# Optimization experiments

Hardware: AMD Instinct MI355X
Metric: run time of the kernel (lower is better)

## Reference

```python
import jax, jax.numpy as jnp
import numpy as np
from jax import lax

S = 101; MAX_LEN = 100; MIN_LEN = 5; NEG = -1e4

def _build_constraints():
    t = np.zeros((S, S), bool)
    t[0, 0] = True; t[0, 1] = True
    for i in range(1, MAX_LEN):
        if i < MAX_LEN - 1:
            t[i, i + 1] = True
        if i >= MIN_LEN - 1:
            t[i, MAX_LEN] = True
    t[MAX_LEN - 1, MAX_LEN - 1] = True; t[MAX_LEN - 1, MAX_LEN] = True
    t[MAX_LEN, 0] = True; t[MAX_LEN, 1] = True
    s = np.ones(S, bool)
    e = np.zeros(S, bool); e[0] = True; e[MAX_LEN] = True
    return jnp.array(t), jnp.array(s), jnp.array(e)

T_ALLOW, S_ALLOW, E_ALLOW = _build_constraints()

def pos_encoding(L, D):
    pos = jnp.arange(L, dtype=jnp.float32)[:, None]
    div = jnp.exp(jnp.arange(0, D, 2, dtype=jnp.float32) * (-np.log(10000.0) / D))
    ang = pos * div
    return jnp.stack([jnp.sin(ang), jnp.cos(ang)], -1).reshape(L, D)

def layernorm(x, g, b, eps=1e-5):
    m = jnp.mean(x, -1, keepdims=True)
    v = jnp.var(x, -1, keepdims=True)
    return (x - m) / jnp.sqrt(v + eps) * g + b

def conv1d(x, w, b):
    # x: (B,C,L), w: (O,I,K), 'same' padding
    k = w.shape[-1]
    y = lax.conv_general_dilated(x, w, (1,), [(k // 2, k // 2)], dimension_numbers=("NCH", "OIH", "NCH"))
    return y + b[None, :, None]

def lstm(x, Wih, Whh, bih, bhh, reverse):
    # x: (B,L,F). PyTorch gate order i,f,g,o.
    B = x.shape[0]; H = Whh.shape[1]
    xs = jnp.swapaxes(x, 0, 1) @ Wih.T + (bih + bhh)  # (L,B,4H)
    def step(carry, xt):
        h, c = carry
        g = xt + h @ Whh.T
        i, f, gg, o = jnp.split(g, 4, axis=-1)
        c = jax.nn.sigmoid(f) * c + jax.nn.sigmoid(i) * jnp.tanh(gg)
        h = jax.nn.sigmoid(o) * jnp.tanh(c)
        return (h, c), h
    h0 = jnp.zeros((B, H), x.dtype)
    _, hs = lax.scan(step, (h0, h0), xs, reverse=reverse)
    return jnp.swapaxes(hs, 0, 1)

def crf_marginals(emis, trans, start, end):
    # forward-backward in log space; mask is all ones (full length)
    ex = jnp.swapaxes(emis, 0, 1)  # (L,B,S)
    a0 = start + ex[0]
    def fstep(a, e):
        a2 = jax.nn.logsumexp(a[:, :, None] + trans[None], axis=1) + e
        return a2, a2
    _, al = lax.scan(fstep, a0, ex[1:])
    alphas = jnp.concatenate([a0[None], al], 0)  # (L,B,S)
    logZ = jax.nn.logsumexp(alphas[-1] + end, axis=-1)  # (B,)
    bT = jnp.broadcast_to(end, a0.shape)
    def bstep(b, e):
        b2 = jax.nn.logsumexp(trans[None] + (e + b)[:, None, :], axis=2)
        return b2, b2
    _, bt = lax.scan(bstep, bT, ex[1:], reverse=True)
    betas = jnp.concatenate([bt, bT[None]], 0)
    probs = jax.nn.softmax(alphas + betas, axis=-1)  # logsumexp(alpha+beta)=logZ
    return jnp.swapaxes(probs, 0, 1), logZ

def viterbi(emis, trans, start, end, logZ):
    ex = jnp.swapaxes(emis, 0, 1)  # (L,B,S)
    v0 = start + ex[0]
    def vstep(v, e):
        sc = v[:, :, None] + trans[None]  # (B,S,S)
        return jnp.max(sc, 1) + e, jnp.argmax(sc, 1).astype(jnp.int32)
    vT, ptrs = lax.scan(vstep, v0, ex[1:])
    fin = vT + end
    last = jnp.argmax(fin, -1).astype(jnp.int32)
    best = jnp.max(fin, -1)
    def back(st, p):
        prev = jnp.take_along_axis(p, st[:, None], axis=1)[:, 0]
        return prev, prev
    _, rest = lax.scan(back, last, ptrs, reverse=True)
    path = jnp.concatenate([rest, last[None]], 0)  # (L,B)
    return jnp.swapaxes(path, 0, 1), jnp.exp(best - logZ)

def features_to_emissions(embeddings, W_bneck, b_bneck, ln_g, ln_b, conv1_w, conv1_b, Wih_f, Whh_f, bih_f, bhh_f, Wih_b, Whh_b, bih_b, bhh_b, conv2_w, conv2_b, W_emis, b_emis):
    B, D, L = embeddings.shape
    x = jnp.swapaxes(embeddings, 1, 2) + pos_encoding(L, D)  # (B,L,D)
    x = jax.nn.relu(layernorm(x @ W_bneck + b_bneck, ln_g, ln_b))
    x = jax.nn.relu(conv1d(jnp.swapaxes(x, 1, 2), conv1_w, conv1_b))
    x = jnp.swapaxes(x, 1, 2)  # (B,L,64)
    h = jnp.concatenate([lstm(x, Wih_f, Whh_f, bih_f, bhh_f, False),
                         lstm(x, Wih_b, Whh_b, bih_b, bhh_b, True)], -1)  # (B,L,256)
    feats = jnp.swapaxes(jax.nn.relu(conv1d(jnp.swapaxes(h, 1, 2), conv2_w, conv2_b)), 1, 2)  # (B,L,128)
    e = feats @ W_emis + b_emis  # (B,L,2); propeptide_bias = 0.0
    # _repeat_emissions: state 0 <- label 0, states 1..100 <- label 1
    return jnp.concatenate([e[..., 0:1], jnp.broadcast_to(e[..., 1:2], (B, L, MAX_LEN))], -1)

def setup_inputs():
    key = jax.random.key(0)
    ks = jax.random.split(key, 16)
    B, L, D = 32, 1024, 1536
    C, F, H, NL = 256, 64, 128, 2
    rn = lambda k, sh, s: s * jax.random.normal(k, sh, jnp.float32)
    return {
        "embeddings": jax.random.normal(ks[0], (B, D, L), jnp.float32),
        "mask": jnp.ones((B, L), jnp.int32),
        "top_k": 1,
        "W_bneck": rn(ks[1], (D, C), 0.02), "b_bneck": jnp.zeros((C,)),
        "ln_g": jnp.ones((C,)), "ln_b": jnp.zeros((C,)),
        "conv1_w": rn(ks[2], (F, C, 3), 0.05), "conv1_b": jnp.zeros((F,)),
        "Wih_f": rn(ks[3], (4 * H, F), 0.08), "Whh_f": rn(ks[4], (4 * H, H), 0.08),
        "bih_f": jnp.zeros((4 * H,)), "bhh_f": jnp.zeros((4 * H,)),
        "Wih_b": rn(ks[5], (4 * H, F), 0.08), "Whh_b": rn(ks[6], (4 * H, H), 0.08),
        "bih_b": jnp.zeros((4 * H,)), "bhh_b": jnp.zeros((4 * H,)),
        "conv2_w": rn(ks[7], (2 * F, 2 * H, 5), 0.04), "conv2_b": jnp.zeros((2 * F,)),
        "W_emis": rn(ks[8], (2 * F, NL), 0.1), "b_emis": jnp.zeros((NL,)),
        "crf_trans": rn(ks[9], (S, S), 0.1),
        "crf_start": rn(ks[10], (S,), 0.1),
        "crf_end": rn(ks[11], (S,), 0.1),
    }

def reference(embeddings, mask, top_k, W_bneck, b_bneck, ln_g, ln_b, conv1_w, conv1_b, Wih_f, Whh_f, bih_f, bhh_f, Wih_b, Whh_b, bih_b, bhh_b, conv2_w, conv2_b, W_emis, b_emis, crf_trans, crf_start, crf_end):
    # mask is all-ones -> packed LSTM == plain LSTM; top_k == 1 Viterbi.
    emis = features_to_emissions(embeddings, W_bneck, b_bneck, ln_g, ln_b, conv1_w, conv1_b, Wih_f, Whh_f, bih_f, bhh_f, Wih_b, Whh_b, bih_b, bhh_b, conv2_w, conv2_b, W_emis, b_emis)
    trans = jnp.where(T_ALLOW, crf_trans, NEG)
    start = jnp.where(S_ALLOW, crf_start, NEG)
    end = jnp.where(E_ALLOW, crf_end, NEG)
    probs, logZ = crf_marginals(emis, trans, start, end)
    paths, path_probs = viterbi(emis, trans, start, end, logZ)
    return probs, paths, path_probs
```

## Files before the change

kernel.cpp:

```cpp
#include <hip/hip_runtime.h>
#include <cstdint>
#include <cstddef>

#define BB 32
#define LL 1024
#define DD 1536
#define SS 101
#define NEGV (-1e4f)
#define NINF (-1e30f)
#define L2E 1.4426950408889634f
#define LN2 0.6931471805599453f

#define NPE   (1024*1536)
#define NX2   (32768*256)
#define NX3   (32768*64)
#define NG    (32768*512)
#define NF2   (32768*128)
#define NEM   (32768*101)

#define OFF_PE    0
#define OFF_X2    (OFF_PE + NPE)
#define OFF_X3    (OFF_X2 + NX2)
#define OFF_GF    (OFF_X3 + NX3)
#define OFF_GB    (OFF_GF + NG)
#define OFF_F2    (OFF_GF)
#define OFF_EMIS  (OFF_GF + NF2)
#define OFF_ALPHA (OFF_EMIS + NEM)
#define OFF_LOGZ  (OFF_ALPHA + NEM)
#define OFF_VBEST (OFF_LOGZ + 64)
#define OFF_WT_F  (OFF_GB + NG)
#define OFF_WT_B  (OFF_WT_F + 32768)
#define OFF_BS_F  (OFF_WT_B + 32768)
#define OFF_BS_B  (OFF_BS_F + 512)
#define OFF_W1R   (OFF_BS_B + 512)
#define OFF_W2R   (OFF_W1R + 49152)

#define LDS_BARRIER asm volatile("s_waitcnt lgkmcnt(0)\ns_barrier" ::: "memory")

__global__ __launch_bounds__(256)
void prep_k(const float* __restrict__ Wihf, const float* __restrict__ Wihb,
            const float* __restrict__ bihf, const float* __restrict__ bhhf,
            const float* __restrict__ bihb, const float* __restrict__ bhhb,
            const float* __restrict__ w1, const float* __restrict__ w2,
            float* __restrict__ ws)
{
  int idx = blockIdx.x * 256 + threadIdx.x;
  if (idx < NPE) {
    int k = idx >> 10, l = idx & 1023;
    int j2 = (k >> 1) * 2;
    float freq = expf((float)j2 * (-9.210340371976184f / 1536.f));
    float ang = (float)l * freq;
    ws[OFF_PE + idx] = (k & 1) ? cosf(ang) : sinf(ang);
    return;
  }
  idx -= NPE;
  if (idx < 32768) { int k = idx >> 9, n = idx & 511; ws[OFF_WT_F + idx] = Wihf[n*64 + k]; return; }
  idx -= 32768;
  if (idx < 32768) { int k = idx >> 9, n = idx & 511; ws[OFF_WT_B + idx] = Wihb[n*64 + k]; return; }
  idx -= 32768;
  if (idx < 512) { ws[OFF_BS_F + idx] = bihf[idx] + bhhf[idx]; return; }
  idx -= 512;
  if (idx < 512) { ws[OFF_BS_B + idx] = bihb[idx] + bhhb[idx]; return; }
  idx -= 512;
  if (idx < 49152) {
    int f = idx & 63, tc = idx >> 6;
    int t = tc >> 8, c = tc & 255;
    ws[OFF_W1R + idx] = w1[(f*256 + c)*3 + t];
    return;
  }
  idx -= 49152;
  if (idx < 163840) {
    int f = idx & 127, tc = idx >> 7;
    int t = tc >> 8, c = tc & 255;
    ws[OFF_W2R + idx] = w2[(f*256 + c)*5 + t];
  }
}

template<int BM, int BN, int AMODE, int PADT, bool RELU>
__global__ __launch_bounds__(256)
void gemm_tpl(const float* __restrict__ Ap, const float* __restrict__ Bp,
              const float* __restrict__ biasp, float* __restrict__ Cp,
              const float* __restrict__ PEp, const float* __restrict__ EMBp,
              int M, int N, int K, int lda)
{
  constexpr int BK = 16;
  __shared__ __align__(16) float As[BK][BM + 4];
  __shared__ __align__(16) float Bs[BK][BN];
  constexpr int TX = BN / 8, TY = BM / 8;
  const int tid = threadIdx.x;
  const int tx = tid % TX, ty = tid / TX;
  const int m0 = blockIdx.x * BM;
  const int n0 = blockIdx.y * BN;
  float acc[8][8];
  #pragma unroll
  for (int i = 0; i < 8; i++)
    #pragma unroll
    for (int j = 0; j < 8; j++) acc[i][j] = 0.f;

  for (int k0 = 0; k0 < K; k0 += BK) {
    if constexpr (AMODE == 0) {
      #pragma unroll
      for (int i = 0; i < (BK*BM)/256; ++i) {
        int e = tid + i*256;
        int ml = e % BM, kk = e / BM;
        int row = m0 + ml; int b = row >> 10; int l = row & 1023;
        int k = k0 + kk;
        As[kk][ml] = EMBp[((size_t)b*DD + k)*LL + l] + PEp[(size_t)k*LL + l];
      }
    } else {
      #pragma unroll
      for (int i = 0; i < (BK*BM)/256; ++i) {
        int e = tid + i*256;
        int kk = e % BK, ml = e / BK;
        int row = m0 + ml; int k = k0 + kk;
        float v;
        if constexpr (AMODE == 1) {
          v = Ap[(size_t)row*lda + k];
        } else {
          int c = k & 255, t = k >> 8;
          int l = row & 1023, sl = l + t - PADT;
          v = ((unsigned)sl < 1024u) ? Ap[(size_t)(row + t - PADT)*lda + c] : 0.f;
        }
        As[kk][ml] = v;
      }
    }
    #pragma unroll
    for (int i = 0; i < (BK*BN)/256; ++i) {
      int e = tid + i*256;
      int nl = e % BN, kk = e / BN;
      Bs[kk][nl] = Bp[(size_t)(k0+kk)*N + n0 + nl];
    }
    __syncthreads();
    #pragma unroll
    for (int k = 0; k < BK; ++k) {
      float4 a0 = *(const float4*)&As[k][ty*4];
      float4 a1 = *(const float4*)&As[k][BM/2 + ty*4];
      float4 b0 = *(const float4*)&Bs[k][tx*4];
      float4 b1 = *(const float4*)&Bs[k][BN/2 + tx*4];
      float av[8] = {a0.x,a0.y,a0.z,a0.w,a1.x,a1.y,a1.z,a1.w};
      float bv[8] = {b0.x,b0.y,b0.z,b0.w,b1.x,b1.y,b1.z,b1.w};
      #pragma unroll
      for (int i = 0; i < 8; i++)
        #pragma unroll
        for (int j = 0; j < 8; j++) acc[i][j] += av[i]*bv[j];
    }
    __syncthreads();
  }
  float4 bias0 = *(const float4*)&biasp[n0 + tx*4];
  float4 bias1 = *(const float4*)&biasp[n0 + BN/2 + tx*4];
  float bn[8] = {bias0.x,bias0.y,bias0.z,bias0.w,bias1.x,bias1.y,bias1.z,bias1.w};
  #pragma unroll
  for (int i = 0; i < 8; i++) {
    int r = m0 + ((i < 4) ? (ty*4 + i) : (BM/2 + ty*4 + i - 4));
    float o[8];
    #pragma unroll
    for (int j = 0; j < 8; j++) {
      float v = acc[i][j] + bn[j];
      o[j] = RELU ? fmaxf(v, 0.f) : v;
    }
    *(float4*)&Cp[(size_t)r*N + n0 + tx*4] = make_float4(o[0],o[1],o[2],o[3]);
    *(float4*)&Cp[(size_t)r*N + n0 + BN/2 + tx*4] = make_float4(o[4],o[5],o[6],o[7]);
  }
}

__global__ __launch_bounds__(256)
void ln_relu_k(float* __restrict__ X, const float* __restrict__ g, const float* __restrict__ bt)
{
  const int lane = threadIdx.x & 63, wv = threadIdx.x >> 6;
  const size_t row = (size_t)blockIdx.x * 4 + wv;
  float4 v = *(const float4*)&X[row*256 + lane*4];
  float s = v.x + v.y + v.z + v.w;
  float q = v.x*v.x + v.y*v.y + v.z*v.z + v.w*v.w;
  #pragma unroll
  for (int d = 1; d < 64; d <<= 1) { s += __shfl_xor(s, d); q += __shfl_xor(q, d); }
  float mean = s * (1.f/256.f);
  float var = q * (1.f/256.f) - mean*mean;
  float inv = 1.f / sqrtf(var + 1e-5f);
  float4 gg = *(const float4*)&g[lane*4];
  float4 bb = *(const float4*)&bt[lane*4];
  float4 o;
  o.x = fmaxf(0.f, (v.x-mean)*inv*gg.x + bb.x);
  o.y = fmaxf(0.f, (v.y-mean)*inv*gg.y + bb.y);
  o.z = fmaxf(0.f, (v.z-mean)*inv*gg.z + bb.z);
  o.w = fmaxf(0.f, (v.w-mean)*inv*gg.w + bb.w);
  *(float4*)&X[row*256 + lane*4] = o;
}

__device__ __forceinline__ float fast_sigmoid(float x){
  return 1.f / (1.f + exp2f(-x * L2E));
}
__device__ __forceinline__ float fast_tanh(float x){
  return 1.f - 2.f / (exp2f(x * (2.f * L2E)) + 1.f);
}

__global__ __launch_bounds__(512)
void lstm_k(const float* __restrict__ GF, const float* __restrict__ GB,
            const float* __restrict__ WhhF, const float* __restrict__ WhhB,
            float* __restrict__ Hcat)
{
  const int dir = blockIdx.y;
  const int b = blockIdx.x;
  const int j = threadIdx.x;
  const float* G = dir ? GB : GF;
  const float* Whh = dir ? WhhB : WhhF;
  float w[128];
  #pragma unroll
  for (int i = 0; i < 32; ++i) {
    float4 t4 = *(const float4*)&Whh[(size_t)j*128 + i*4];
    w[4*i+0] = t4.x; w[4*i+1] = t4.y; w[4*i+2] = t4.z; w[4*i+3] = t4.w;
  }
  __shared__ __align__(16) float hs[128];
  __shared__ float gs[512];
  if (j < 128) hs[j] = 0.f;
  float c = 0.f;
  const size_t gbase = (size_t)b * LL * 512 + j;
  float gcur = G[gbase + (size_t)(dir ? 1023 : 0) * 512];
  __syncthreads();
  for (int step = 0; step < LL; ++step) {
    const int l = dir ? (1023 - step) : step;
    float gnext = 0.f;
    if (step + 1 < LL) {
      const int ln = dir ? (1022 - step) : (step + 1);
      gnext = G[gbase + (size_t)ln * 512];
    }
    #pragma unroll
    for (int k = 0; k < 128; ++k)
      asm volatile("" : "+v"(w[k]));
    float ac0 = gcur, ac1 = 0.f, ac2 = 0.f, ac3 = 0.f;
    #pragma unroll
    for (int i = 0; i < 8; ++i) {
      float4 h0 = *(const float4*)&hs[16*i];
      float4 h1 = *(const float4*)&hs[16*i + 4];
      float4 h2 = *(const float4*)&hs[16*i + 8];
      float4 h3 = *(const float4*)&hs[16*i + 12];
      ac0 += h0.x*w[16*i]    + h0.y*w[16*i+1]  + h0.z*w[16*i+2]  + h0.w*w[16*i+3];
      ac1 += h1.x*w[16*i+4]  + h1.y*w[16*i+5]  + h1.z*w[16*i+6]  + h1.w*w[16*i+7];
      ac2 += h2.x*w[16*i+8]  + h2.y*w[16*i+9]  + h2.z*w[16*i+10] + h2.w*w[16*i+11];
      ac3 += h3.x*w[16*i+12] + h3.y*w[16*i+13] + h3.z*w[16*i+14] + h3.w*w[16*i+15];
    }
    float acc = (ac0 + ac1) + (ac2 + ac3);
    float gv = ((j >> 7) == 2) ? fast_tanh(acc) : fast_sigmoid(acc);
    gs[j] = gv;
    LDS_BARRIER;
    if (j < 128) {
      float ig = gs[j], fg = gs[128+j], g2 = gs[256+j], og = gs[384+j];
      c = fg*c + ig*g2;
      float hh = og * fast_tanh(c);
      hs[j] = hh;
      Hcat[((size_t)b*LL + l)*256 + (dir << 7) + j] = hh;
    }
    LDS_BARRIER;
    gcur = gnext;
  }
}

__device__ __forceinline__ float wave_sum_f(float v){
  #pragma unroll
  for (int d = 1; d < 64; d <<= 1) v += __shfl_xor(v, d);
  return v;
}
__device__ __forceinline__ float wave_max_f(float v){
  #pragma unroll
  for (int d = 1; d < 64; d <<= 1) v = fmaxf(v, __shfl_xor(v, d));
  return v;
}
__device__ __forceinline__ float rdlanef(float v, int l){
  union { float f; int i; } u; u.f = v;
  u.i = __builtin_amdgcn_readlane(u.i, l);
  return u.f;
}
__device__ __forceinline__ float lse2f(float x, float y){
  float mx = fmaxf(x, y), mn = fminf(x, y);
  return mx + log2f(1.f + exp2f((mn - mx) * L2E)) * LN2;
}

__global__ __launch_bounds__(256)
void emis_k(const float* __restrict__ F2, const float* __restrict__ W,
            const float* __restrict__ bias, float* __restrict__ EM)
{
  const int lane = threadIdx.x & 63;
  const size_t m = (size_t)blockIdx.x * 4 + (threadIdx.x >> 6);
  float f1 = F2[m*128 + lane], f2 = F2[m*128 + 64 + lane];
  float e0 = f1*W[lane*2]   + f2*W[(64+lane)*2];
  float e1 = f1*W[lane*2+1] + f2*W[(64+lane)*2+1];
  e0 = wave_sum_f(e0) + bias[0];
  e1 = wave_sum_f(e1) + bias[1];
  float* row = EM + m*SS;
  row[lane] = (lane == 0) ? e0 : e1;
  if (lane < 37) row[64 + lane] = e1;
}

__global__ __launch_bounds__(64)
void crf1_k(const float* __restrict__ EM, const float* __restrict__ T,
            const float* __restrict__ startv, const float* __restrict__ endv,
            float* __restrict__ AL, float* __restrict__ LOGZ,
            float* __restrict__ paths, float* __restrict__ vbest)
{
  __shared__ unsigned int lptr[LL];
  const int lane = threadIdx.x;
  const int s1 = lane, s2 = 64 + lane;
  const bool has2 = lane < 37;
  float ta1, tb1 = 0.f, tc1 = NINF, ta2 = 0.f, tb2 = 0.f, tc2 = NINF;
  if (s1 == 0)      { ta1 = T[0]; tb1 = T[100*101 + 0]; }
  else if (s1 == 1) { ta1 = T[1]; tb1 = T[100*101 + 1]; }
  else ta1 = T[(s1-1)*101 + s1];
  if (s1 >= 4) tc1 = T[s1*101 + 100];
  if (has2) {
    if (s2 <= 98) ta2 = T[(s2-1)*101 + s2];
    else if (s2 == 99) { ta2 = T[98*101 + 99]; tb2 = T[99*101 + 99]; }
    if (s2 <= 99) tc2 = T[s2*101 + 100];
  }

  if (blockIdx.x < 32) {
    const int b = blockIdx.x;
    const float* E = EM + (size_t)b*LL*SS;
    float* A = AL + (size_t)b*LL*SS;
    float a1 = startv[s1] + E[s1];
    float a2 = has2 ? (startv[s2] + E[s2]) : NINF;
    A[s1] = a1;
    if (has2) A[s2] = a2;
    float M;
    {
      float v1 = a1 + tc1;
      float v2 = a2 + tc2;
      M = wave_max_f(fmaxf(v1, v2));
    }
    auto fstep = [&](int l, float e1, float e2) {
      float v1 = a1 + tc1;
      float v2 = a2 + tc2;
      float p = exp2f((v1 - M) * L2E) + exp2f((v2 - M) * L2E);
      p = fmaxf(wave_sum_f(p), 1e-37f);
      float lse100 = M + log2f(p) * LN2;
      float a1m1 = __shfl_up(a1, 1);
      float a2m1 = __shfl_up(a2, 1);
      float a1t  = rdlanef(a1, 63);
      float a0s  = rdlanef(a1, 0);
      float a100 = rdlanef(a2, 36);
      float n1 = (s1 <= 1) ? lse2f(a0s + ta1, a100 + tb1) : (a1m1 + ta1);
      float n2;
      if (s2 == 64) n2 = a1t + ta2;
      else if (s2 <= 98) n2 = a2m1 + ta2;
      else if (s2 == 99) n2 = lse2f(a2m1 + ta2, a2 + tb2);
      else n2 = lse100;
      a1 = n1 + e1;
      a2 = has2 ? (n2 + e2) : NINF;
      float* Ar = A + (size_t)l*SS;
      Ar[s1] = a1;
      if (has2) Ar[s2] = a2;
      M = lse100;
    };
    int l = 1;
    for (; l + 3 < LL; l += 4) {
      float e1a[4], e2a[4];
      #pragma unroll
      for (int u = 0; u < 4; ++u) {
        const float* e = E + (size_t)(l+u)*SS;
        e1a[u] = e[s1]; e2a[u] = has2 ? e[s2] : 0.f;
      }
      #pragma unroll
      for (int u = 0; u < 4; ++u) fstep(l+u, e1a[u], e2a[u]);
    }
    for (; l < LL; ++l) {
      const float* e = E + (size_t)l*SS;
      fstep(l, e[s1], has2 ? e[s2] : 0.f);
    }
    float w1 = a1 + ((s1 == 0) ? endv[0] : NEGV);
    float w2 = has2 ? (a2 + ((s2 == 100) ? endv[100] : NEGV)) : NINF;
    float Mx = wave_max_f(fmaxf(w1, w2));
    float P = wave_sum_f(exp2f((w1 - Mx) * L2E) + exp2f((w2 - Mx) * L2E));
    if (lane == 0) LOGZ[b] = Mx + log2f(P) * LN2;
  } else {
    const int b = blockIdx.x - 32;
    const float* E = EM + (size_t)b*LL*SS;
    float v1 = startv[s1] + E[s1];
    float v2 = has2 ? (startv[s2] + E[s2]) : NINF;
    auto vstep = [&](int l, float e1, float e2) {
      float c1 = v1 + tc1;
      float c2 = v2 + tc2;
      float Mx = wave_max_f(fmaxf(c1, c2));
      unsigned long long m1 = __ballot(c1 == Mx);
      int bi;
      if (m1 != 0ULL) bi = __ffsll((unsigned long long)m1) - 1;
      else bi = 64 + __ffsll((unsigned long long)__ballot(c2 == Mx)) - 1;
      float v1m1 = __shfl_up(v1, 1);
      float v2m1 = __shfl_up(v2, 1);
      float v1t  = rdlanef(v1, 63);
      float v0s  = rdlanef(v1, 0);
      float v100 = rdlanef(v2, 36);
      float n1; int p1i;
      if (s1 <= 1) {
        float x0 = v0s + ta1, x1 = v100 + tb1;
        if (x1 > x0) { n1 = x1; p1i = 100; } else { n1 = x0; p1i = 0; }
      } else { n1 = v1m1 + ta1; p1i = s1 - 1; }
      float n2 = NINF; int p2i = 0;
      if (has2) {
        if (s2 == 64) { n2 = v1t + ta2; p2i = 63; }
        else if (s2 <= 98) { n2 = v2m1 + ta2; p2i = s2 - 1; }
        else if (s2 == 99) {
          float x98 = v2m1 + ta2, x99 = v2 + tb2;
          if (x99 > x98) { n2 = x99; p2i = 99; } else { n2 = x98; p2i = 98; }
        } else { n2 = Mx; p2i = bi; }
      }
      v1 = n1 + e1;
      v2 = has2 ? (n2 + e2) : NINF;
      int q0   = __builtin_amdgcn_readlane(p1i, 0);
      int q1   = __builtin_amdgcn_readlane(p1i, 1);
      int q99  = __builtin_amdgcn_readlane(p2i, 35);
      int q100 = __builtin_amdgcn_readlane(p2i, 36);
      if (lane == 0)
        lptr[l] = (unsigned)q0 | ((unsigned)q1 << 8) | ((unsigned)q99 << 16) | ((unsigned)q100 << 24);
    };
    int l = 1;
    for (; l + 3 < LL; l += 4) {
      float e1a[4], e2a[4];
      #pragma unroll
      for (int u = 0; u < 4; ++u) {
        const float* e = E + (size_t)(l+u)*SS;
        e1a[u] = e[s1]; e2a[u] = has2 ? e[s2] : 0.f;
      }
      #pragma unroll
      for (int u = 0; u < 4; ++u) vstep(l+u, e1a[u], e2a[u]);
    }
    for (; l < LL; ++l) {
      const float* e = E + (size_t)l*SS;
      vstep(l, e[s1], has2 ? e[s2] : 0.f);
    }
    float w1 = v1 + ((s1 == 0) ? endv[0] : NEGV);
    float w2 = has2 ? (v2 + ((s2 == 100) ? endv[100] : NEGV)) : NINF;
    float Mx = wave_max_f(fmaxf(w1, w2));
    unsigned long long m1 = __ballot(w1 == Mx);
    int last;
    if (m1 != 0ULL) last = __ffsll((unsigned long long)m1) - 1;
    else last = 64 + __ffsll((unsigned long long)__ballot(w2 == Mx)) - 1;
    if (lane == 0) vbest[b] = Mx;
    __syncthreads();
    float* po = paths + (size_t)b*LL;
    int st = last;
    for (int ch = 15; ch >= 0; --ch) {
      unsigned pk = lptr[ch*64 + lane];
      int myval = 0;
      #pragma unroll 1
      for (int j = 63; j >= 0; --j) {
        int t = ch*64 + j;
        if (t >= 1) {
          unsigned pp = __shfl((int)pk, j);
          int prev;
          if (st >= 2 && st <= 98) prev = st - 1;
          else if (st == 0)  prev = (int)(pp & 0xffu);
          else if (st == 1)  prev = (int)((pp >> 8) & 0xffu);
          else if (st == 99) prev = (int)((pp >> 16) & 0xffu);
          else               prev = (int)((pp >> 24) & 0xffu);
          if (j == lane) myval = prev;
          st = prev;
        }
      }
      int ii = ch*64 + lane;
      if (ii >= 1) po[ii - 1] = (float)myval;
    }
    if (lane == 0) po[1023] = (float)last;
  }
}

__global__ __launch_bounds__(64)
void crf_bwd_k(const float* __restrict__ EM, const float* __restrict__ AL,
               const float* __restrict__ T, const float* __restrict__ endv,
               float* __restrict__ U)
{
  const int b = blockIdx.x, lane = threadIdx.x;
  const int s1 = lane, s2 = 64 + lane;
  const bool has2 = lane < 37;
  const float* E = EM + (size_t)b*LL*SS;
  const float* A = AL + (size_t)b*LL*SS;
  float* PR = U + (size_t)b*LL*SS;
  float tn1 = T[s1*101 + s1 + 1];
  float tj1 = (s1 >= 4) ? T[s1*101 + 100] : 0.f;
  float tn2 = (has2 && s2 <= 99) ? T[s2*101 + s2 + 1] : 0.f;
  float tj2 = (has2 && s2 <= 98) ? T[s2*101 + 100] : 0.f;
  float t00 = T[0];
  float t9999 = T[99*101 + 99];
  float t100_0 = T[100*101 + 0], t100_1 = T[100*101 + 1];
  float b1 = (s1 == 0) ? endv[0] : NEGV;
  float b2 = has2 ? ((s2 == 100) ? endv[100] : NEGV) : NINF;
  PR[(size_t)1023*SS + s1] = A[(size_t)1023*SS + s1] + b1;
  if (has2) PR[(size_t)1023*SS + s2] = A[(size_t)1023*SS + s2] + b2;
  auto bstep = [&](int l, float e1, float e2, float a1r, float a2r) {
    float u1 = e1 + b1;
    float u2 = has2 ? (e2 + b2) : NINF;
    float un1 = __shfl_down(u1, 1);
    float un2 = __shfl_down(u2, 1);
    float u64v = rdlanef(u2, 0);
    float u99  = rdlanef(u2, 35);
    float u100 = rdlanef(u2, 36);
    float u0s  = rdlanef(u1, 0);
    float u1s  = rdlanef(u1, 1);
    float nb1;
    if (s1 == 0) nb1 = lse2f(t00 + u0s, tn1 + u1s);
    else if (s1 <= 3) nb1 = tn1 + un1;
    else if (s1 <= 62) nb1 = lse2f(tn1 + un1, tj1 + u100);
    else nb1 = lse2f(tn1 + u64v, tj1 + u100);
    float nb2 = NINF;
    if (has2) {
      if (s2 <= 98) nb2 = lse2f(tn2 + un2, tj2 + u100);
      else if (s2 == 99) nb2 = lse2f(t9999 + u99, tn2 + u100);
      else nb2 = lse2f(t100_0 + u0s, t100_1 + u1s);
    }
    b1 = nb1; b2 = has2 ? nb2 : NINF;
    PR[(size_t)(l-1)*SS + s1] = a1r + b1;
    if (has2) PR[(size_t)(l-1)*SS + s2] = a2r + b2;
  };
  int l = 1023;
  for (; l >= 4; l -= 4) {
    float e1a[4], e2a[4], a1a[4], a2a[4];
    #pragma unroll
    for (int u = 0; u < 4; ++u) {
      const float* e = E + (size_t)(l-u)*SS;
      const float* a = A + (size_t)(l-1-u)*SS;
      e1a[u] = e[s1]; e2a[u] = has2 ? e[s2] : 0.f;
      a1a[u] = a[s1]; a2a[u] = has2 ? a[s2] : 0.f;
    }
    #pragma unroll
    for (int u = 0; u < 4; ++u) bstep(l-u, e1a[u], e2a[u], a1a[u], a2a[u]);
  }
  for (; l >= 1; --l) {
    const float* e = E + (size_t)l*SS;
    const float* a = A + (size_t)(l-1)*SS;
    bstep(l, e[s1], has2 ? e[s2] : 0.f, a[s1], has2 ? a[s2] : 0.f);
  }
}

__global__ __launch_bounds__(256)
void crf_norm_k(float* __restrict__ PR, const float* __restrict__ vbest,
                const float* __restrict__ LOGZ, float* __restrict__ pprobs)
{
  const int lane = threadIdx.x & 63;
  const size_t m = (size_t)blockIdx.x * 4 + (threadIdx.x >> 6);
  float* row = PR + m*SS;
  float w1 = row[lane];
  float w2 = (lane < 37) ? row[64 + lane] : NINF;
  float M = wave_max_f(fmaxf(w1, w2));
  float p1 = exp2f((w1 - M) * L2E);
  float p2 = (lane < 37) ? exp2f((w2 - M) * L2E) : 0.f;
  float Z = wave_sum_f(p1 + p2);
  float rz = 1.f / Z;
  row[lane] = p1 * rz;
  if (lane < 37) row[64 + lane] = p2 * rz;
  if (blockIdx.x == 0 && threadIdx.x < 32)
    pprobs[threadIdx.x] = exp2f((vbest[threadIdx.x] - LOGZ[threadIdx.x]) * L2E);
}

extern "C" void kernel_launch(void* const* d_in, const int* in_sizes, int n_in,
                              void* d_out, int out_size, void* d_ws, size_t ws_size,
                              hipStream_t stream)
{
  (void)in_sizes; (void)n_in; (void)out_size; (void)ws_size;
  const float* emb      = (const float*)d_in[0];
  const float* W_bneck  = (const float*)d_in[3];
  const float* b_bneck  = (const float*)d_in[4];
  const float* ln_g     = (const float*)d_in[5];
  const float* ln_b     = (const float*)d_in[6];
  const float* conv1_w  = (const float*)d_in[7];
  const float* conv1_b  = (const float*)d_in[8];
  const float* Wih_f    = (const float*)d_in[9];
  const float* Whh_f    = (const float*)d_in[10];
  const float* bih_f    = (const float*)d_in[11];
  const float* bhh_f    = (const float*)d_in[12];
  const float* Wih_b    = (const float*)d_in[13];
  const float* Whh_b    = (const float*)d_in[14];
  const float* bih_b    = (const float*)d_in[15];
  const float* bhh_b    = (const float*)d_in[16];
  const float* conv2_w  = (const float*)d_in[17];
  const float* conv2_b  = (const float*)d_in[18];
  const float* W_emis   = (const float*)d_in[19];
  const float* b_emis   = (const float*)d_in[20];
  const float* crf_trans= (const float*)d_in[21];
  const float* crf_start= (const float*)d_in[22];
  const float* crf_end  = (const float*)d_in[23];
  float* ws = (float*)d_ws;
  float* out = (float*)d_out;

  dim3 b256(256);
  prep_k<<<dim3(7236), b256, 0, stream>>>(Wih_f, Wih_b, bih_f, bhh_f, bih_b, bhh_b,
                                          conv1_w, conv2_w, ws);
  gemm_tpl<64,256,0,0,false><<<dim3(512,1), b256, 0, stream>>>(
      nullptr, W_bneck, b_bneck, ws + OFF_X2, ws + OFF_PE, emb, 32768, 256, 1536, 0);
  ln_relu_k<<<dim3(8192), b256, 0, stream>>>(ws + OFF_X2, ln_g, ln_b);
  gemm_tpl<256,64,2,1,true><<<dim3(128,1), b256, 0, stream>>>(
      ws + OFF_X2, ws + OFF_W1R, conv1_b, ws + OFF_X3, nullptr, nullptr, 32768, 64, 768, 256);
  gemm_tpl<64,256,1,0,false><<<dim3(512,2), b256, 0, stream>>>(
      ws + OFF_X3, ws + OFF_WT_F, ws + OFF_BS_F, ws + OFF_GF, nullptr, nullptr, 32768, 512, 64, 64);
  gemm_tpl<64,256,1,0,false><<<dim3(512,2), b256, 0, stream>>>(
      ws + OFF_X3, ws + OFF_WT_B, ws + OFF_BS_B, ws + OFF_GB, nullptr, nullptr, 32768, 512, 64, 64);
  lstm_k<<<dim3(32,2), dim3(512), 0, stream>>>(ws + OFF_GF, ws + OFF_GB, Whh_f, Whh_b, ws + OFF_X2);
  gemm_tpl<128,128,2,2,true><<<dim3(256,1), b256, 0, stream>>>(
      ws + OFF_X2, ws + OFF_W2R, conv2_b, ws + OFF_F2, nullptr, nullptr, 32768, 128, 1280, 256);
  emis_k<<<dim3(8192), b256, 0, stream>>>(ws + OFF_F2, W_emis, b_emis, ws + OFF_EMIS);
  crf1_k<<<dim3(64), dim3(64), 0, stream>>>(ws + OFF_EMIS, crf_trans, crf_start, crf_end,
                                            ws + OFF_ALPHA, ws + OFF_LOGZ,
                                            out + 3309568, ws + OFF_VBEST);
  crf_bwd_k<<<dim3(32), dim3(64), 0, stream>>>(ws + OFF_EMIS, ws + OFF_ALPHA,
                                               crf_trans, crf_end, out);
  crf_norm_k<<<dim3(8192), b256, 0, stream>>>(out, ws + OFF_VBEST, ws + OFF_LOGZ,
                                              out + 3342336);
}
```

Measured before the change: 3.172 ms.

## Split LSTM recurrent dot product across two threads per gate row

The LSTM recurrence kernel now launches 1024 threads per block instead of 512. Each pair of threads computes half of a 128-wide hidden-state dot product and combines the halves with a lane shuffle. This halves the per-thread serial FMA chain and the weight registers held per thread, aiming to cut per-step latency on the sequential critical path. In exchange, block-wide barriers now span twice as many waves, and half the threads sit idle during the gate activation.

After: 3.575 ms. +12.7%, slower.

```diff
diff --git a/kernel.cpp b/kernel.cpp
--- a/kernel.cpp
+++ b/kernel.cpp
@@ -193,61 +193,68 @@
   return 1.f - 2.f / (exp2f(x * (2.f * L2E)) + 1.f);
 }
 
-__global__ __launch_bounds__(512)
+__global__ __launch_bounds__(1024)
 void lstm_k(const float* __restrict__ GF, const float* __restrict__ GB,
             const float* __restrict__ WhhF, const float* __restrict__ WhhB,
             float* __restrict__ Hcat)
 {
   const int dir = blockIdx.y;
   const int b = blockIdx.x;
-  const int j = threadIdx.x;
+  const int t = threadIdx.x;
+  const int j = t >> 1;
+  const int half = t & 1;
   const float* G = dir ? GB : GF;
   const float* Whh = dir ? WhhB : WhhF;
-  float w[128];
+  float w[64];
   #pragma unroll
-  for (int i = 0; i < 32; ++i) {
-    float4 t4 = *(const float4*)&Whh[(size_t)j*128 + i*4];
+  for (int i = 0; i < 16; ++i) {
+    float4 t4 = *(const float4*)&Whh[(size_t)j*128 + half*64 + i*4];
     w[4*i+0] = t4.x; w[4*i+1] = t4.y; w[4*i+2] = t4.z; w[4*i+3] = t4.w;
   }
+  #pragma unroll
+  for (int k = 0; k < 64; ++k)
+    asm volatile("" : "+v"(w[k]));
   __shared__ __align__(16) float hs[128];
   __shared__ float gs[512];
-  if (j < 128) hs[j] = 0.f;
+  if (t < 128) hs[t] = 0.f;
   float c = 0.f;
   const size_t gbase = (size_t)b * LL * 512 + j;
-  float gcur = G[gbase + (size_t)(dir ? 1023 : 0) * 512];
+  float gcur = (half == 0) ? G[gbase + (size_t)(dir ? 1023 : 0) * 512] : 0.f;
   __syncthreads();
   for (int step = 0; step < LL; ++step) {
     const int l = dir ? (1023 - step) : step;
     float gnext = 0.f;
-    if (step + 1 < LL) {
+    if (half == 0 && step + 1 < LL) {
       const int ln = dir ? (1022 - step) : (step + 1);
       gnext = G[gbase + (size_t)ln * 512];
     }
+    const float* hbase = &hs[half * 64];
+    float ac0 = 0.f, ac1 = 0.f, ac2 = 0.f, ac3 = 0.f;
     #pragma unroll
-    for (int k = 0; k < 128; ++k)
-      asm volatile("" : "+v"(w[k]));
-    float ac0 = gcur, ac1 = 0.f, ac2 = 0.f, ac3 = 0.f;
-    #pragma unroll
-    for (int i = 0; i < 8; ++i) {
-      float4 h0 = *(const float4*)&hs[16*i];
-      float4 h1 = *(const float4*)&hs[16*i + 4];
-      float4 h2 = *(const float4*)&hs[16*i + 8];
-      float4 h3 = *(const float4*)&hs[16*i + 12];
+    for (int i = 0; i < 4; ++i) {
+      float4 h0 = *(const float4*)&hbase[16*i];
+      float4 h1 = *(const float4*)&hbase[16*i + 4];
+      float4 h2 = *(const float4*)&hbase[16*i + 8];
+      float4 h3 = *(const float4*)&hbase[16*i + 12];
       ac0 += h0.x*w[16*i]    + h0.y*w[16*i+1]  + h0.z*w[16*i+2]  + h0.w*w[16*i+3];
       ac1 += h1.x*w[16*i+4]  + h1.y*w[16*i+5]  + h1.z*w[16*i+6]  + h1.w*w[16*i+7];
       ac2 += h2.x*w[16*i+8]  + h2.y*w[16*i+9]  + h2.z*w[16*i+10] + h2.w*w[16*i+11];
       ac3 += h3.x*w[16*i+12] + h3.y*w[16*i+13] + h3.z*w[16*i+14] + h3.w*w[16*i+15];
     }
-    float acc = (ac0 + ac1) + (ac2 + ac3);
-    float gv = ((j >> 7) == 2) ? fast_tanh(acc) : fast_sigmoid(acc);
-    gs[j] = gv;
+    float part = (ac0 + ac1) + (ac2 + ac3);
+    part += __shfl_xor(part, 1);
+    if (half == 0) {
+      float acc = gcur + part;
+      float gv = ((j >> 7) == 2) ? fast_tanh(acc) : fast_sigmoid(acc);
+      gs[j] = gv;
+    }
     LDS_BARRIER;
-    if (j < 128) {
-      float ig = gs[j], fg = gs[128+j], g2 = gs[256+j], og = gs[384+j];
+    if (t < 128) {
+      float ig = gs[t], fg = gs[128+t], g2 = gs[256+t], og = gs[384+t];
       c = fg*c + ig*g2;
       float hh = og * fast_tanh(c);
-      hs[j] = hh;
-      Hcat[((size_t)b*LL + l)*256 + (dir << 7) + j] = hh;
+      hs[t] = hh;
+      Hcat[((size_t)b*LL + l)*256 + (dir << 7) + t] = hh;
     }
     LDS_BARRIER;
     gcur = gnext;
@@ -590,7 +597,7 @@
       ws + OFF_X3, ws + OFF_WT_F, ws + OFF_BS_F, ws + OFF_GF, nullptr, nullptr, 32768, 512, 64, 64);
   gemm_tpl<64,256,1,0,false><<<dim3(512,2), b256, 0, stream>>>(
       ws + OFF_X3, ws + OFF_WT_B, ws + OFF_BS_B, ws + OFF_GB, nullptr, nullptr, 32768, 512, 64, 64);
-  lstm_k<<<dim3(32,2), dim3(512), 0, stream>>>(ws + OFF_GF, ws + OFF_GB, Whh_f, Whh_b, ws + OFF_X2);
+  lstm_k<<<dim3(32,2), dim3(1024), 0, stream>>>(ws + OFF_GF, ws + OFF_GB, Whh_f, Whh_b, ws + OFF_X2);
   gemm_tpl<128,128,2,2,true><<<dim3(256,1), b256, 0, stream>>>(
       ws + OFF_X2, ws + OFF_W2R, conv2_b, ws + OFF_F2, nullptr, nullptr, 32768, 128, 1280, 256);
   emis_k<<<dim3(8192), b256, 0, stream>>>(ws + OFF_F2, W_emis, b_emis, ws + OFF_EMIS);
```
